# Kernel optimization log

Hardware: AMD Instinct MI355X
Metric: run time of the kernel (lower is better)

## Reference

```python
import jax, jax.numpy as jnp
import numpy as np

B, L, D = 8, 4096, 1024
EPS = 1e-6


def setup_inputs() -> dict:
    key = jax.random.key(0)
    k1, k2, k3 = jax.random.split(key, 3)
    x = jax.random.normal(k1, (B, L, D), dtype=jnp.float32)
    # torch.nn.Linear default init ~ U(-1/sqrt(d), 1/sqrt(d)); scaled normal is fine for a reference
    w_in = jax.random.normal(k2, (3 * D, D), dtype=jnp.float32) * (D ** -0.5)
    w_out = jax.random.normal(k3, (D, D), dtype=jnp.float32) * (D ** -0.5)
    scale = jnp.ones((D,), dtype=jnp.float32)
    return {"x": x, "w_in": w_in, "w_out": w_out, "scale": scale}


def reference(x, w_in, w_out, scale):
    residual = x
    # RMSNorm: ||x||_2 * d^{-1/2}
    norm = jnp.linalg.norm(x, axis=-1, keepdims=True) * (x.shape[-1] ** -0.5)
    xn = scale * x / (norm + EPS)
    # proj_in: Linear(d, 3d, bias=False) -> chunk into g, v, f
    gvf = jnp.einsum('bld,ed->ble', xn, w_in)  # [B, L, 3D]
    g, v, f = jnp.split(gvf, 3, axis=-1)
    g = jax.nn.sigmoid(g)
    f = jax.nn.sigmoid(f - 1.0)

    # sequential gated linear recurrence: h_t = f_t * h_{t-1} + (1 - f_t) * v_t
    def step(h, fv):
        ft, vt = fv  # each [B, D]
        h = ft * h + (1.0 - ft) * vt
        return h, h

    h0 = jnp.zeros((x.shape[0], x.shape[2]), dtype=x.dtype)
    _, h_seq = jax.lax.scan(step, h0, (jnp.swapaxes(f, 0, 1), jnp.swapaxes(v, 0, 1)))
    h_seq = jnp.swapaxes(h_seq, 0, 1)  # [B, L, D]

    out = g * h_seq
    return residual + jnp.einsum('bld,ed->ble', out, w_out)
```

## Files before the change

kernel.cpp:

```cpp
#include <hip/hip_runtime.h>
#include <cstdint>
#include <cstddef>

typedef unsigned short u16;
typedef __attribute__((ext_vector_type(8))) short short8;
typedef __attribute__((ext_vector_type(4))) float floatx4;
typedef __attribute__((ext_vector_type(4))) unsigned short ushort4v;

constexpr int D_ = 1024;
constexpr int B_ = 8;
constexpr int L_ = 4096;
constexpr int M_ = B_ * L_;
constexpr int NCHUNK = 64;
constexpr int CLEN = L_ / NCHUNK;
constexpr float EPS_ = 1e-6f;
constexpr size_t WIN_ELEMS = (size_t)3 * D_ * D_;
constexpr size_t WOUT_ELEMS = (size_t)D_ * D_;

__device__ __forceinline__ float bf2f(u16 b) {
    union { unsigned u; float f; } x; x.u = ((unsigned)b) << 16; return x.f;
}
__device__ __forceinline__ u16 f2bf(float f) {
    union { float f; unsigned u; } x; x.f = f;
    unsigned r = x.u + 0x7fffu + ((x.u >> 16) & 1u);
    return (u16)(r >> 16);
}
__device__ __forceinline__ float sigmoidf_(float x) {
    return 1.f / (1.f + __expf(-x));
}
__device__ __forceinline__ short8 cvt8(const float* __restrict__ p) {
    float4 a = *(const float4*)p;
    float4 b = *(const float4*)(p + 4);
    short8 o;
    o[0] = (short)f2bf(a.x); o[1] = (short)f2bf(a.y);
    o[2] = (short)f2bf(a.z); o[3] = (short)f2bf(a.w);
    o[4] = (short)f2bf(b.x); o[5] = (short)f2bf(b.y);
    o[6] = (short)f2bf(b.z); o[7] = (short)f2bf(b.w);
    return o;
}
__device__ __forceinline__ void gload16(const void* g, void* l) {
    __builtin_amdgcn_global_load_lds((const __attribute__((address_space(1))) void*)g,
                                     (__attribute__((address_space(3))) void*)l, 16, 0, 0);
}

__global__ __launch_bounds__(256) void prep_xn_kernel(const float* __restrict__ x,
                                                      const float* __restrict__ scale,
                                                      u16* __restrict__ xn) {
    const int row = blockIdx.x;
    const int t = threadIdx.x;
    const float* xr = x + (size_t)row * D_;
    float4 xv = ((const float4*)xr)[t];
    float ss = xv.x * xv.x + xv.y * xv.y + xv.z * xv.z + xv.w * xv.w;
#pragma unroll
    for (int m = 32; m >= 1; m >>= 1) ss += __shfl_xor(ss, m, 64);
    __shared__ float red[4];
    const int wave = t >> 6, lane = t & 63;
    if (lane == 0) red[wave] = ss;
    __syncthreads();
    float tot = red[0] + red[1] + red[2] + red[3];
    float inv = 1.f / (sqrtf(tot * (1.f / D_)) + EPS_);
    float4 sv = ((const float4*)scale)[t];
    ushort4v o;
    o[0] = f2bf(xv.x * inv * sv.x);
    o[1] = f2bf(xv.y * inv * sv.y);
    o[2] = f2bf(xv.z * inv * sv.z);
    o[3] = f2bf(xv.w * inv * sv.w);
    ((ushort4v*)(xn + (size_t)row * D_))[t] = o;
}

__global__ __launch_bounds__(256) void prep_w_kernel(const float* __restrict__ w_in,
                                                     const float* __restrict__ w_out,
                                                     u16* __restrict__ w_in_bf,
                                                     u16* __restrict__ w_out_bf) {
    size_t i8 = ((size_t)blockIdx.x * 256 + threadIdx.x) * 8;
    if (i8 < WIN_ELEMS) {
        *(short8*)(w_in_bf + i8) = cvt8(w_in + i8);
    } else {
        size_t j = i8 - WIN_ELEMS;
        *(short8*)(w_out_bf + j) = cvt8(w_out + j);
    }
}

__device__ __forceinline__ void gemm_core(const u16* __restrict__ gA,
                                          const u16* __restrict__ gB,
                                          int m0, int n0,
                                          u16* As, u16* Bs,
                                          floatx4 (&acc)[4][4]) {
    const int t = threadIdx.x;
    const int wave = t >> 6, lane = t & 63;
    const int wm0 = (wave >> 1) * 64, wn0 = (wave & 1) * 64;
    const int l15 = lane & 15, quad = lane >> 4;

#pragma unroll
    for (int i = 0; i < 4; i++)
#pragma unroll
        for (int j = 0; j < 4; j++) { floatx4 z = {0.f, 0.f, 0.f, 0.f}; acc[i][j] = z; }

    const int srow = lane >> 2;
    const int scol = (lane & 3) * 8;
    const int rb0 = wave * 2;

    const u16* gA0 = gA + (size_t)(m0 + rb0 * 16 + srow) * 1024 + scol;
    const u16* gB0 = gB + (size_t)(n0 + rb0 * 16 + srow) * 1024 + scol;
    u16* lA0 = As + rb0 * 512;
    u16* lB0 = Bs + rb0 * 512;

    for (int k0 = 0; k0 < 1024; k0 += 32) {
        __syncthreads();
        gload16(gA0 + k0, lA0);
        gload16(gA0 + k0 + 16 * 1024, lA0 + 512);
        gload16(gB0 + k0, lB0);
        gload16(gB0 + k0 + 16 * 1024, lB0 + 512);
        __syncthreads();
        short8 af[4], bfr[4];
#pragma unroll
        for (int mt = 0; mt < 4; mt++)
            af[mt] = *(const short8*)&As[(wm0 + mt * 16 + l15) * 32 + quad * 8];
#pragma unroll
        for (int nt = 0; nt < 4; nt++)
            bfr[nt] = *(const short8*)&Bs[(wn0 + nt * 16 + l15) * 32 + quad * 8];
#pragma unroll
        for (int mt = 0; mt < 4; mt++)
#pragma unroll
            for (int nt = 0; nt < 4; nt++)
                acc[mt][nt] = __builtin_amdgcn_mfma_f32_16x16x32_bf16(
                    af[mt], bfr[nt], acc[mt][nt], 0, 0, 0);
    }
}

__global__ __launch_bounds__(256) void gemm1_kernel(const u16* __restrict__ xn,
                                                    const u16* __restrict__ w_in,
                                                    u16* __restrict__ g_buf,
                                                    u16* __restrict__ v_buf,
                                                    u16* __restrict__ f_buf) {
    __shared__ __align__(16) u16 As[128 * 32];
    __shared__ __align__(16) u16 Bs[128 * 32];
    const int m0 = blockIdx.y * 128;
    const int n0 = blockIdx.x * 128;
    floatx4 acc[4][4];
    gemm_core(xn, w_in, m0, n0, As, Bs, acc);

    const int t = threadIdx.x;
    const int wave = t >> 6, lane = t & 63;
    const int wm0 = (wave >> 1) * 64, wn0 = (wave & 1) * 64;
    const int l15 = lane & 15, quad = lane >> 4;
    const int plane = n0 >> 10;
    const int dcol0 = n0 & 1023;
    u16* dst = (plane == 0) ? g_buf : ((plane == 1) ? v_buf : f_buf);
#pragma unroll
    for (int mt = 0; mt < 4; mt++) {
#pragma unroll
        for (int r = 0; r < 4; r++) {
            int m = m0 + wm0 + mt * 16 + quad * 4 + r;
#pragma unroll
            for (int nt = 0; nt < 4; nt++) {
                int d = dcol0 + wn0 + nt * 16 + l15;
                float val = acc[mt][nt][r];
                if (plane == 0) val = sigmoidf_(val);
                else if (plane == 2) val = sigmoidf_(val - 1.f);
                dst[(size_t)m * 1024 + d] = f2bf(val);
            }
        }
    }
}

__global__ __launch_bounds__(256) void gemm2_kernel(const u16* __restrict__ op,
                                                    const u16* __restrict__ w_out,
                                                    const float* __restrict__ xres,
                                                    float* __restrict__ out) {
    __shared__ __align__(16) u16 As[128 * 32];
    __shared__ __align__(16) u16 Bs[128 * 32];
    const int m0 = blockIdx.y * 128;
    const int n0 = blockIdx.x * 128;
    floatx4 acc[4][4];
    gemm_core(op, w_out, m0, n0, As, Bs, acc);

    const int t = threadIdx.x;
    const int wave = t >> 6, lane = t & 63;
    const int wm0 = (wave >> 1) * 64, wn0 = (wave & 1) * 64;
    const int l15 = lane & 15, quad = lane >> 4;
#pragma unroll
    for (int mt = 0; mt < 4; mt++) {
#pragma unroll
        for (int r = 0; r < 4; r++) {
            int m = m0 + wm0 + mt * 16 + quad * 4 + r;
#pragma unroll
            for (int nt = 0; nt < 4; nt++) {
                int n = n0 + wn0 + nt * 16 + l15;
                size_t idx = (size_t)m * 1024 + n;
                out[idx] = acc[mt][nt][r] + xres[idx];
            }
        }
    }
}

__global__ __launch_bounds__(256) void scan1_kernel(const u16* __restrict__ f_buf,
                                                    const u16* __restrict__ v_buf,
                                                    float* __restrict__ Aarr,
                                                    float* __restrict__ Barr) {
    const int wid = blockIdx.x * 4 + (threadIdx.x >> 6);
    const int lane = threadIdx.x & 63;
    const int b = wid >> 10;
    const int rem = wid & 1023;
    const int c = rem >> 4;
    const int db = (rem & 15) * 64 + lane;
    float A = 1.f, Bv = 0.f;
    size_t base = ((size_t)b * L_ + c * CLEN) * D_ + db;
#pragma unroll 4
    for (int tt = 0; tt < CLEN; tt++) {
        float fv = bf2f(f_buf[base + (size_t)tt * D_]);
        float vv = bf2f(v_buf[base + (size_t)tt * D_]);
        A *= fv;
        Bv = fv * Bv + (1.f - fv) * vv;
    }
    size_t sidx = ((size_t)b * NCHUNK + c) * D_ + db;
    Aarr[sidx] = A;
    Barr[sidx] = Bv;
}

__global__ __launch_bounds__(256) void scan2_kernel(const float* __restrict__ Aarr,
                                                    const float* __restrict__ Barr,
                                                    float* __restrict__ hin) {
    const int id = blockIdx.x * 256 + threadIdx.x;
    const int b = id >> 10, d = id & 1023;
    float h = 0.f;
    for (int c = 0; c < NCHUNK; c++) {
        size_t idx = ((size_t)b * NCHUNK + c) * D_ + d;
        hin[idx] = h;
        h = Aarr[idx] * h + Barr[idx];
    }
}

__global__ __launch_bounds__(256) void scan3_kernel(const u16* __restrict__ f_buf,
                                                    const u16* __restrict__ v_buf,
                                                    u16* g_io,
                                                    const float* __restrict__ hin) {
    const int wid = blockIdx.x * 4 + (threadIdx.x >> 6);
    const int lane = threadIdx.x & 63;
    const int b = wid >> 10;
    const int rem = wid & 1023;
    const int c = rem >> 4;
    const int db = (rem & 15) * 64 + lane;
    size_t base = ((size_t)b * L_ + c * CLEN) * D_ + db;
    float h = hin[((size_t)b * NCHUNK + c) * D_ + db];
#pragma unroll 4
    for (int tt = 0; tt < CLEN; tt++) {
        size_t idx = base + (size_t)tt * D_;
        float fv = bf2f(f_buf[idx]);
        float vv = bf2f(v_buf[idx]);
        float gv = bf2f(g_io[idx]);
        h = fv * h + (1.f - fv) * vv;
        g_io[idx] = f2bf(gv * h);
    }
}

extern "C" void kernel_launch(void* const* d_in, const int* in_sizes, int n_in,
                              void* d_out, int out_size, void* d_ws, size_t ws_size,
                              hipStream_t stream) {
    const float* x     = (const float*)d_in[0];
    const float* w_in  = (const float*)d_in[1];
    const float* w_out = (const float*)d_in[2];
    const float* scale = (const float*)d_in[3];
    float* out = (float*)d_out;

    u16* f_buf = (u16*)d_out;
    u16* v_buf = (u16*)d_out + (size_t)M_ * D_;

    char* ws = (char*)d_ws;
    const size_t PLANE = (size_t)M_ * D_ * sizeof(u16);
    u16* xn    = (u16*)ws;
    u16* g_buf = (u16*)(ws + PLANE);
    u16* w_in_bf  = (u16*)(ws + 2 * PLANE);
    u16* w_out_bf = w_in_bf + WIN_ELEMS;
    float* Aarr = (float*)(ws + 2 * PLANE + (WIN_ELEMS + WOUT_ELEMS) * sizeof(u16));
    float* Barr = Aarr + (size_t)B_ * NCHUNK * D_;
    float* hin  = Barr + (size_t)B_ * NCHUNK * D_;

    prep_xn_kernel<<<M_, 256, 0, stream>>>(x, scale, xn);
    prep_w_kernel<<<(int)((WIN_ELEMS + WOUT_ELEMS) / 8 / 256), 256, 0, stream>>>(
        w_in, w_out, w_in_bf, w_out_bf);
    gemm1_kernel<<<dim3(3 * D_ / 128, M_ / 128), 256, 0, stream>>>(
        xn, w_in_bf, g_buf, v_buf, f_buf);
    scan1_kernel<<<(B_ * NCHUNK * 16) / 4, 256, 0, stream>>>(f_buf, v_buf, Aarr, Barr);
    scan2_kernel<<<(B_ * D_) / 256, 256, 0, stream>>>(Aarr, Barr, hin);
    scan3_kernel<<<(B_ * NCHUNK * 16) / 4, 256, 0, stream>>>(f_buf, v_buf, g_buf, hin);
    gemm2_kernel<<<dim3(D_ / 128, M_ / 128), 256, 0, stream>>>(g_buf, w_out_bf, x, out);
}
```

Baseline: 768.6 us.

## Rewrite GEMM core as 256x256 tiles with double-buffered, swizzled LDS pipeline

Both GEMMs now use 256x256 output tiles with 512 threads (8 waves) and a K-step of 64. Global-to-LDS loads are double-buffered and interleaved with MFMA quarters, using explicit barriers, waitcnt and setprio. An XOR swizzle on the LDS layout is meant to avoid bank conflicts. The aim is more data reuse per tile and hiding memory latency behind MFMA work. In exchange it uses far more registers and LDS per block and relies on fragile hand-tuned vmcnt accounting.

```diff
diff --git a/kernel.cpp b/kernel.cpp
--- a/kernel.cpp
+++ b/kernel.cpp
@@ -16,6 +16,7 @@
 constexpr float EPS_ = 1e-6f;
 constexpr size_t WIN_ELEMS = (size_t)3 * D_ * D_;
 constexpr size_t WOUT_ELEMS = (size_t)D_ * D_;
+constexpr int NT_K = 16;
 
 __device__ __forceinline__ float bf2f(u16 b) {
     union { unsigned u; float f; } x; x.u = ((unsigned)b) << 16; return x.f;
@@ -81,113 +82,170 @@
     }
 }
 
-__device__ __forceinline__ void gemm_core(const u16* __restrict__ gA,
-                                          const u16* __restrict__ gB,
-                                          int m0, int n0,
-                                          u16* As, u16* Bs,
-                                          floatx4 (&acc)[4][4]) {
+
+#define STAGE_A_(buf, half, koff) do { \
+    const u16* g_ = gA0 + (koff) + (half) * 65536; \
+    u16* l_ = (buf) + ((half) * 64 + iw) * 64; \
+    gload16(g_, l_); gload16(g_ + 131072, l_ + 8192); } while (0)
+#define STAGE_B_(buf, half, koff) do { \
+    const u16* g_ = gB0 + (koff) + (half) * 32768; \
+    u16* l_ = (buf) + (rBw + (half) * 32) * 64; \
+    gload16(g_, l_); gload16(g_ + 131072, l_ + 8192); } while (0)
+#define BARRIER_() do { __builtin_amdgcn_sched_barrier(0); \
+    __builtin_amdgcn_s_barrier(); \
+    __builtin_amdgcn_sched_barrier(0); } while (0)
+#define LDA4_(mlo) do { \
+    _Pragma("unroll") for (int m_ = 0; m_ < 4; ++m_) { \
+      int o_ = aOff + ((mlo) + m_) * 2048; \
+      af[m_][0] = *(const short8*)((const char*)curA + o_); \
+      af[m_][1] = *(const short8*)((const char*)curA + (o_ ^ 64)); } } while (0)
+#define LDB2_(nlo) do { \
+    _Pragma("unroll") for (int n_ = 0; n_ < 2; ++n_) { \
+      int o_ = bOff + ((nlo) + n_) * 2048; \
+      bfv[n_][0] = *(const short8*)((const char*)curB + o_); \
+      bfv[n_][1] = *(const short8*)((const char*)curB + (o_ ^ 64)); } } while (0)
+#define MFMA_Q_(mlo, nlo) do { \
+    __builtin_amdgcn_s_setprio(1); \
+    _Pragma("unroll") for (int m_ = 0; m_ < 4; ++m_) \
+    _Pragma("unroll") for (int n_ = 0; n_ < 2; ++n_) \
+    _Pragma("unroll") for (int k_ = 0; k_ < 2; ++k_) \
+      acc[(mlo) + m_][(nlo) + n_] = __builtin_amdgcn_mfma_f32_16x16x32_bf16( \
+          af[m_][k_], bfv[n_][k_], acc[(mlo) + m_][(nlo) + n_], 0, 0, 0); \
+    __builtin_amdgcn_s_setprio(0); } while (0)
+
+__device__ __forceinline__ void tile_step(int tt, u16* curA, u16* curB, u16* othA, u16* othB,
+                                          const u16* gA0, const u16* gB0, int iw, int rBw,
+                                          int aOff, int bOff, floatx4 (&acc)[8][4]) {
+    short8 af[4][2], bfv[2][2];
+    const int k1 = (tt + 1) * 64, k2 = (tt + 2) * 64;
+    const bool s1 = (tt + 1 < NT_K), s2 = (tt + 2 < NT_K);
+    LDA4_(0); LDB2_(0);
+    if (s1) STAGE_A_(othA, 1, k1);
+    BARRIER_();
+    MFMA_Q_(0, 0);
+    BARRIER_();
+    LDB2_(2);
+    if (s1) STAGE_B_(othB, 1, k1);
+    BARRIER_();
+    MFMA_Q_(0, 2);
+    BARRIER_();
+    LDA4_(4); LDB2_(0);
+    if (s2) STAGE_A_(curA, 0, k2);
+    BARRIER_();
+    MFMA_Q_(4, 0);
+    BARRIER_();
+    LDB2_(2);
+    if (s2) STAGE_B_(curB, 0, k2);
+    BARRIER_();
+    MFMA_Q_(4, 2);
+    if (s2)      { asm volatile("s_waitcnt vmcnt(4)" ::: "memory"); }
+    else if (s1) { asm volatile("s_waitcnt vmcnt(0)" ::: "memory"); }
+    BARRIER_();
+}
+
+__device__ __forceinline__ void gemm256_core(const u16* __restrict__ gA,
+                                             const u16* __restrict__ gB,
+                                             int m0, int n0,
+                                             u16* __restrict__ As, u16* __restrict__ Bs,
+                                             floatx4 (&acc)[8][4]) {
     const int t = threadIdx.x;
-    const int wave = t >> 6, lane = t & 63;
-    const int wm0 = (wave >> 1) * 64, wn0 = (wave & 1) * 64;
+    const int wid = t >> 6, lane = t & 63;
+    const int wr = wid >> 2, wc = wid & 3;
     const int l15 = lane & 15, quad = lane >> 4;
-
-#pragma unroll
-    for (int i = 0; i < 4; i++)
+    const int jrow = lane >> 3, jc = lane & 7;
+    const int swz = ((jc ^ (jrow & 7)) << 3);
+    const u16* gA0 = gA + (size_t)(m0 + wid * 8 + jrow) * 1024 + swz;
+    const int i0 = wid * 8 + jrow;
+    const int rB0 = ((i0 >> 5) << 6) + (i0 & 31);
+    const u16* gB0 = gB + (size_t)(n0 + rB0) * 1024 + swz;
+    const int iw = wid * 8;
+    const int rBw = ((iw >> 5) << 6) + (iw & 31);
+    const int c0 = (quad * 16) ^ ((l15 & 7) << 4);
+    const int aOff = (wr * 128 + l15) * 128 + c0;
+    const int bOff = (wc * 64 + l15) * 128 + c0;
+
+#pragma unroll
+    for (int i = 0; i < 8; i++)
 #pragma unroll
         for (int j = 0; j < 4; j++) { floatx4 z = {0.f, 0.f, 0.f, 0.f}; acc[i][j] = z; }
 
-    const int srow = lane >> 2;
-    const int scol = (lane & 3) * 8;
-    const int rb0 = wave * 2;
-
-    const u16* gA0 = gA + (size_t)(m0 + rb0 * 16 + srow) * 1024 + scol;
-    const u16* gB0 = gB + (size_t)(n0 + rb0 * 16 + srow) * 1024 + scol;
-    u16* lA0 = As + rb0 * 512;
-    u16* lB0 = Bs + rb0 * 512;
-
-    for (int k0 = 0; k0 < 1024; k0 += 32) {
-        __syncthreads();
-        gload16(gA0 + k0, lA0);
-        gload16(gA0 + k0 + 16 * 1024, lA0 + 512);
-        gload16(gB0 + k0, lB0);
-        gload16(gB0 + k0 + 16 * 1024, lB0 + 512);
-        __syncthreads();
-        short8 af[4], bfr[4];
-#pragma unroll
-        for (int mt = 0; mt < 4; mt++)
-            af[mt] = *(const short8*)&As[(wm0 + mt * 16 + l15) * 32 + quad * 8];
-#pragma unroll
-        for (int nt = 0; nt < 4; nt++)
-            bfr[nt] = *(const short8*)&Bs[(wn0 + nt * 16 + l15) * 32 + quad * 8];
-#pragma unroll
-        for (int mt = 0; mt < 4; mt++)
-#pragma unroll
-            for (int nt = 0; nt < 4; nt++)
-                acc[mt][nt] = __builtin_amdgcn_mfma_f32_16x16x32_bf16(
-                    af[mt], bfr[nt], acc[mt][nt], 0, 0, 0);
-    }
-}
-
-__global__ __launch_bounds__(256) void gemm1_kernel(const u16* __restrict__ xn,
-                                                    const u16* __restrict__ w_in,
-                                                    u16* __restrict__ g_buf,
-                                                    u16* __restrict__ v_buf,
-                                                    u16* __restrict__ f_buf) {
-    __shared__ __align__(16) u16 As[128 * 32];
-    __shared__ __align__(16) u16 Bs[128 * 32];
-    const int m0 = blockIdx.y * 128;
-    const int n0 = blockIdx.x * 128;
-    floatx4 acc[4][4];
-    gemm_core(xn, w_in, m0, n0, As, Bs, acc);
+    STAGE_A_(As, 0, 0); STAGE_A_(As, 1, 0);
+    STAGE_B_(Bs, 0, 0); STAGE_B_(Bs, 1, 0);
+    STAGE_A_(As + 16384, 0, 64);
+    STAGE_B_(Bs + 16384, 0, 64);
+    asm volatile("s_waitcnt vmcnt(4)" ::: "memory");
+    BARRIER_();
+
+#pragma unroll 1
+    for (int tt = 0; tt < NT_K; tt += 2) {
+        tile_step(tt,     As,         Bs,         As + 16384, Bs + 16384,
+                  gA0, gB0, iw, rBw, aOff, bOff, acc);
+        tile_step(tt + 1, As + 16384, Bs + 16384, As,         Bs,
+                  gA0, gB0, iw, rBw, aOff, bOff, acc);
+    }
+}
+
+__global__ __launch_bounds__(512, 2) void gemm1_kernel(const u16* __restrict__ xn,
+                                                       const u16* __restrict__ w_in,
+                                                       u16* __restrict__ g_buf,
+                                                       u16* __restrict__ v_buf,
+                                                       u16* __restrict__ f_buf) {
+    __shared__ __align__(16) u16 As[2 * 16384];
+    __shared__ __align__(16) u16 Bs[2 * 16384];
+    const int m0 = blockIdx.y * 256;
+    const int n0 = blockIdx.x * 256;
+    floatx4 acc[8][4];
+    gemm256_core(xn, w_in, m0, n0, As, Bs, acc);
 
     const int t = threadIdx.x;
-    const int wave = t >> 6, lane = t & 63;
-    const int wm0 = (wave >> 1) * 64, wn0 = (wave & 1) * 64;
+    const int wid = t >> 6, lane = t & 63;
+    const int wr = wid >> 2, wc = wid & 3;
     const int l15 = lane & 15, quad = lane >> 4;
     const int plane = n0 >> 10;
-    const int dcol0 = n0 & 1023;
+    const int dcol0 = (n0 & 1023) + wc * 64;
     u16* dst = (plane == 0) ? g_buf : ((plane == 1) ? v_buf : f_buf);
-#pragma unroll
-    for (int mt = 0; mt < 4; mt++) {
+    const int mrow0 = m0 + wr * 128 + quad * 4;
+#pragma unroll
+    for (int mt = 0; mt < 8; mt++) {
 #pragma unroll
         for (int r = 0; r < 4; r++) {
-            int m = m0 + wm0 + mt * 16 + quad * 4 + r;
+            int m = mrow0 + mt * 16 + r;
 #pragma unroll
             for (int nt = 0; nt < 4; nt++) {
-                int d = dcol0 + wn0 + nt * 16 + l15;
                 float val = acc[mt][nt][r];
                 if (plane == 0) val = sigmoidf_(val);
                 else if (plane == 2) val = sigmoidf_(val - 1.f);
-                dst[(size_t)m * 1024 + d] = f2bf(val);
+                dst[(size_t)m * 1024 + dcol0 + nt * 16 + l15] = f2bf(val);
             }
         }
     }
 }
 
-__global__ __launch_bounds__(256) void gemm2_kernel(const u16* __restrict__ op,
-                                                    const u16* __restrict__ w_out,
-                                                    const float* __restrict__ xres,
-                                                    float* __restrict__ out) {
-    __shared__ __align__(16) u16 As[128 * 32];
-    __shared__ __align__(16) u16 Bs[128 * 32];
-    const int m0 = blockIdx.y * 128;
-    const int n0 = blockIdx.x * 128;
-    floatx4 acc[4][4];
-    gemm_core(op, w_out, m0, n0, As, Bs, acc);
+__global__ __launch_bounds__(512, 2) void gemm2_kernel(const u16* __restrict__ op,
+                                                       const u16* __restrict__ w_out,
+                                                       const float* __restrict__ xres,
+                                                       float* __restrict__ out) {
+    __shared__ __align__(16) u16 As[2 * 16384];
+    __shared__ __align__(16) u16 Bs[2 * 16384];
+    const int m0 = blockIdx.y * 256;
+    const int n0 = blockIdx.x * 256;
+    floatx4 acc[8][4];
+    gemm256_core(op, w_out, m0, n0, As, Bs, acc);
 
     const int t = threadIdx.x;
-    const int wave = t >> 6, lane = t & 63;
-    const int wm0 = (wave >> 1) * 64, wn0 = (wave & 1) * 64;
+    const int wid = t >> 6, lane = t & 63;
+    const int wr = wid >> 2, wc = wid & 3;
     const int l15 = lane & 15, quad = lane >> 4;
-#pragma unroll
-    for (int mt = 0; mt < 4; mt++) {
+    const int ncol0 = n0 + wc * 64;
+    const int mrow0 = m0 + wr * 128 + quad * 4;
+#pragma unroll
+    for (int mt = 0; mt < 8; mt++) {
 #pragma unroll
         for (int r = 0; r < 4; r++) {
-            int m = m0 + wm0 + mt * 16 + quad * 4 + r;
+            int m = mrow0 + mt * 16 + r;
 #pragma unroll
             for (int nt = 0; nt < 4; nt++) {
-                int n = n0 + wn0 + nt * 16 + l15;
-                size_t idx = (size_t)m * 1024 + n;
+                size_t idx = (size_t)m * 1024 + ncol0 + nt * 16 + l15;
                 out[idx] = acc[mt][nt][r] + xres[idx];
             }
         }
@@ -279,10 +337,10 @@
     prep_xn_kernel<<<M_, 256, 0, stream>>>(x, scale, xn);
     prep_w_kernel<<<(int)((WIN_ELEMS + WOUT_ELEMS) / 8 / 256), 256, 0, stream>>>(
         w_in, w_out, w_in_bf, w_out_bf);
-    gemm1_kernel<<<dim3(3 * D_ / 128, M_ / 128), 256, 0, stream>>>(
+    gemm1_kernel<<<dim3(3 * D_ / 256, M_ / 256), 512, 0, stream>>>(
         xn, w_in_bf, g_buf, v_buf, f_buf);
     scan1_kernel<<<(B_ * NCHUNK * 16) / 4, 256, 0, stream>>>(f_buf, v_buf, Aarr, Barr);
     scan2_kernel<<<(B_ * D_) / 256, 256, 0, stream>>>(Aarr, Barr, hin);
     scan3_kernel<<<(B_ * NCHUNK * 16) / 4, 256, 0, stream>>>(f_buf, v_buf, g_buf, hin);
-    gemm2_kernel<<<dim3(D_ / 128, M_ / 128), 256, 0, stream>>>(g_buf, w_out_bf, x, out);
-}
+    gemm2_kernel<<<dim3(D_ / 256, M_ / 256), 512, 0, stream>>>(g_buf, w_out_bf, x, out);
+}
```

After: 638.1 us. -17.0%, faster.
